# Optimization experiments

Measured on AMD Instinct MI355X. Metric: run time of the kernel, lower is better.

## Reference

```python
import jax, jax.numpy as jnp
import numpy as np

N = 2048
NODE_DIM = 128
HID = 128
HID2 = max(HID // 2, 4)  # 64
NUM_EDGE_TYPES = 1
TEMPERATURE = 1.0
LN_EPS = 1e-5


def setup_inputs() -> dict:
    key = jax.random.key(0)
    ks = jax.random.split(key, 12)
    s = lambda fan_in: 1.0 / np.sqrt(fan_in)
    inp = {
        "node_features": jax.random.normal(ks[0], (N, NODE_DIM), dtype=jnp.float32),
        # node_transform: Linear(node_dim, hidden)
        "Wt": jax.random.uniform(ks[1], (NODE_DIM, HID), jnp.float32, -s(NODE_DIM), s(NODE_DIM)),
        "bt": jax.random.uniform(ks[2], (HID,), jnp.float32, -s(NODE_DIM), s(NODE_DIM)),
        # edge_mlp Linear(2*hidden, hidden)
        "W1": jax.random.uniform(ks[3], (2 * HID, HID), jnp.float32, -s(2 * HID), s(2 * HID)),
        "b1": jax.random.uniform(ks[4], (HID,), jnp.float32, -s(2 * HID), s(2 * HID)),
        # LayerNorm(hidden)
        "ln_g": jnp.ones((HID,), jnp.float32),
        "ln_b": jnp.zeros((HID,), jnp.float32),
        # Linear(hidden, hidden//2)
        "W2": jax.random.uniform(ks[5], (HID, HID2), jnp.float32, -s(HID), s(HID)),
        "b2": jax.random.uniform(ks[6], (HID2,), jnp.float32, -s(HID), s(HID)),
        # Linear(hidden//2, num_edge_types)
        "W3": jax.random.uniform(ks[7], (HID2, NUM_EDGE_TYPES), jnp.float32, -s(HID2), s(HID2)),
        "b3": jax.random.uniform(ks[8], (NUM_EDGE_TYPES,), jnp.float32, -s(HID2), s(HID2)),
    }
    return inp


def reference(node_features, Wt, bt, W1, b1, ln_g, ln_b, W2, b2, W3, b3):
    n = node_features.shape[0]
    # node transform + relu: [n, hid]
    h = jax.nn.relu(node_features @ Wt + bt)
    # upper-triangular pair indices (i < j), matching the python loop order
    idx_i, idx_j = jnp.triu_indices(n, k=1)
    # gather + concat: [n_pairs, 2*hid]
    pair_feats = jnp.concatenate([h[idx_i], h[idx_j]], axis=1)
    # MLP: linear -> LN -> relu -> (dropout=identity in eval) -> linear -> relu -> linear
    z = pair_feats @ W1 + b1
    mu = jnp.mean(z, axis=-1, keepdims=True)
    var = jnp.mean((z - mu) ** 2, axis=-1, keepdims=True)
    z = (z - mu) * jax.lax.rsqrt(var + LN_EPS) * ln_g + ln_b
    z = jax.nn.relu(z)
    z = jax.nn.relu(z @ W2 + b2)
    logits = z @ W3 + b3  # [n_pairs, 1]
    probs = jax.nn.sigmoid(logits / max(1e-6, TEMPERATURE))
    pair_index = jnp.stack([idx_i, idx_j], axis=0)  # [2, n_pairs]
    p = probs.squeeze(1)
    soft_adj = jnp.zeros((n, n), dtype=probs.dtype)
    soft_adj = soft_adj.at[idx_i, idx_j].set(p).at[idx_j, idx_i].set(p)
    return probs, pair_index, soft_adj
```

## Files before the change

kernel.cpp:

```cpp
#include <hip/hip_runtime.h>
#include <math.h>

#define NN 2048
#define HID 128
#define HID2 64
#define NP ((NN*(NN-1))/2)

typedef _Float16 f16x8 __attribute__((ext_vector_type(8)));
typedef float    f32x4 __attribute__((ext_vector_type(4)));

__global__ __launch_bounds__(128) void precompute_AB(
    const float* __restrict__ X, const float* __restrict__ Wt, const float* __restrict__ bt,
    const float* __restrict__ W1, const float* __restrict__ b1,
    _Float16* __restrict__ Ah, _Float16* __restrict__ Bp,
    float2* __restrict__ sa, float2* __restrict__ sb)
{
    __shared__ float x_s[HID];
    __shared__ float h_s[HID];
    __shared__ float red[2][4];
    const int row = blockIdx.x;
    const int c = threadIdx.x;
    x_s[c] = X[row*HID + c];
    __syncthreads();
    float hc = bt[c];
    #pragma unroll 8
    for (int k = 0; k < HID; ++k) hc = fmaf(x_s[k], Wt[k*HID + c], hc);
    h_s[c] = fmaxf(hc, 0.f);
    __syncthreads();
    float a = b1[c];
    float bsum = 0.f;
    #pragma unroll 8
    for (int k = 0; k < HID; ++k) {
        float hk = h_s[k];
        a    = fmaf(hk, W1[k*HID + c], a);
        bsum = fmaf(hk, W1[(HID + k)*HID + c], bsum);
    }
    const _Float16 ah = (_Float16)a;
    const _Float16 bh = (_Float16)bsum;
    Ah[row*HID + c] = ah;
    {
        const int ks = c >> 5, g4 = (c >> 3) & 3, e = c & 7;
        Bp[(((size_t)(row >> 4)*4 + ks)*64 + g4*16 + (row & 15))*8 + e] = bh;
    }
    const float ar = (float)ah;
    const float br = (float)bh;
    float r0 = ar, r1 = ar*ar, r2 = br, r3 = br*br;
    #pragma unroll
    for (int m = 1; m <= 32; m <<= 1) {
        r0 += __shfl_xor(r0, m); r1 += __shfl_xor(r1, m);
        r2 += __shfl_xor(r2, m); r3 += __shfl_xor(r3, m);
    }
    if ((c & 63) == 0) {
        red[c >> 6][0] = r0; red[c >> 6][1] = r1; red[c >> 6][2] = r2; red[c >> 6][3] = r3;
    }
    __syncthreads();
    if (c == 0) {
        sa[row] = make_float2(red[0][0] + red[1][0], red[0][1] + red[1][1]);
        sb[row] = make_float2(red[0][2] + red[1][2], red[0][3] + red[1][3]);
    }
}

__global__ __launch_bounds__(256) void pack_W2(const float* __restrict__ W2,
                                               const float* __restrict__ ln_g,
                                               const float* __restrict__ ln_b,
                                               _Float16* __restrict__ W2p,
                                               _Float16* __restrict__ ghl,
                                               _Float16* __restrict__ lhl)
{
    const int t = threadIdx.x;
    if (t < HID) { ghl[t] = (_Float16)ln_g[t]; lhl[t] = (_Float16)ln_b[t]; }
    for (int fs = t; fs < 16*64; fs += 256) {
        const int frag = fs >> 6, lane = fs & 63;
        const int ks = frag >> 2, nt = frag & 3;
        const int kbase = ks*32 + (lane >> 4)*8;
        const int col   = nt*16 + (lane & 15);
        #pragma unroll
        for (int e = 0; e < 8; ++e)
            W2p[fs*8 + e] = (_Float16)W2[(kbase + e)*HID2 + col];
    }
}

__global__ __launch_bounds__(256) void fill_pi(float* __restrict__ pi)
{
    const int i = blockIdx.x;
    const size_t off = (size_t)i*(NN-1) - (size_t)i*(i-1)/2;
    const int cnt = NN - 1 - i;
    for (int t = threadIdx.x; t < cnt; t += 256) {
        pi[off + t]      = (float)i;
        pi[NP + off + t] = (float)(i + 1 + t);
    }
}

__global__ __launch_bounds__(256, 3) void pairs_mfma(
    const _Float16* __restrict__ Ah, const _Float16* __restrict__ Bp,
    const float2* __restrict__ sa, const float2* __restrict__ sb,
    const _Float16* __restrict__ ghl, const _Float16* __restrict__ lhl,
    const _Float16* __restrict__ W2p, const float* __restrict__ b2,
    const float* __restrict__ W3, const float* __restrict__ b3,
    float* __restrict__ out)
{
    __shared__ f16x8 w2s[16*64];

    {
        const f16x8* __restrict__ W2v = (const f16x8*)W2p;
        #pragma unroll
        for (int t = 0; t < 4; ++t)
            w2s[t*256 + threadIdx.x] = W2v[t*256 + threadIdx.x];
    }

    int t = blockIdx.x;
    int q = 0, base = 0;
    while (q < 7 && t >= base + 256*(8 - q)) { base += 256*(8 - q); ++q; }
    const int idx = t - base;
    const int den = 8 - q;
    const int i  = (q << 8) + idx / den;
    const int jb = q + idx % den;

    __syncthreads();

    const int w    = threadIdx.x >> 6;
    const int lane = threadIdx.x & 63;
    const int jw0  = (jb << 8) + (w << 6);
    if (jw0 + 63 < i) return;

    const int p16 = lane & 15;
    const int g4  = lane >> 4;

    f16x8 abf[4], gh[4], lh[4];
    #pragma unroll
    for (int ks = 0; ks < 4; ++ks) {
        const int kb = ks*32 + g4*8;
        abf[ks] = *(const f16x8*)(Ah + (size_t)i*HID + kb);
        gh[ks]  = *(const f16x8*)(ghl + kb);
        lh[ks]  = *(const f16x8*)(lhl + kb);
    }
    const float2 sav = sa[i];

    const f16x8* __restrict__ Bpv = (const f16x8*)Bp;

    float parts[4];

    f16x8 bcur[4], bnxt[4];
    {
        const size_t fb = ((size_t)(jw0 >> 4))*4;
        #pragma unroll
        for (int ks = 0; ks < 4; ++ks) bcur[ks] = Bpv[(fb + ks)*64 + lane];
    }

    #pragma unroll
    for (int s = 0; s < 4; ++s) {
        if (s < 3) {
            const size_t fbn = ((size_t)((jw0 + (s+1)*16) >> 4))*4;
            #pragma unroll
            for (int ks = 0; ks < 4; ++ks) bnxt[ks] = Bpv[(fbn + ks)*64 + lane];
        }
        const int j16 = jw0 + s*16;

        f32x4 d0 = (f32x4){0.f,0.f,0.f,0.f};
        f32x4 d1 = (f32x4){0.f,0.f,0.f,0.f};
        f32x4 d2 = (f32x4){0.f,0.f,0.f,0.f};
        f32x4 d3 = (f32x4){0.f,0.f,0.f,0.f};
        d0 = __builtin_amdgcn_mfma_f32_16x16x32_f16(abf[0], bcur[0], d0, 0, 0, 0);
        d1 = __builtin_amdgcn_mfma_f32_16x16x32_f16(abf[1], bcur[1], d1, 0, 0, 0);
        d2 = __builtin_amdgcn_mfma_f32_16x16x32_f16(abf[2], bcur[2], d2, 0, 0, 0);
        d3 = __builtin_amdgcn_mfma_f32_16x16x32_f16(abf[3], bcur[3], d3, 0, 0, 0);

        const float2 sbv = sb[j16 + p16];
        const float dd   = (d0[0] + d1[0]) + (d2[0] + d3[0]);
        const float mu   = (sav.x + sbv.x) * (1.f/HID);
        const float ez2  = (sav.y + sbv.y + 2.f*dd) * (1.f/HID);
        const float rstd = rsqrtf(ez2 - mu*mu + 1e-5f);
        const float v    = -mu * rstd;

        const _Float16 rh = (_Float16)rstd;
        const _Float16 vh = (_Float16)v;
        const f16x8 zero8 = {};

        f32x4 acc[4];
        #pragma unroll
        for (int nt = 0; nt < 4; ++nt) acc[nt] = *(const f32x4*)(b2 + nt*16 + g4*4);

        #pragma unroll
        for (int ks = 0; ks < 4; ++ks) {
            f16x8 z  = abf[ks] + bcur[ks];
            f16x8 qq = z * rh + vh;
            f16x8 af = __builtin_elementwise_max(gh[ks] * qq + lh[ks], zero8);
            #pragma unroll
            for (int nt = 0; nt < 4; ++nt)
                acc[nt] = __builtin_amdgcn_mfma_f32_16x16x32_f16(w2s[(ks*4 + nt)*64 + lane], af, acc[nt], 0, 0, 0);
        }

        float part = 0.f;
        #pragma unroll
        for (int nt = 0; nt < 4; ++nt) {
            f32x4 w3v = *(const f32x4*)(W3 + nt*16 + g4*4);
            #pragma unroll
            for (int r = 0; r < 4; ++r)
                part = fmaf(fmaxf(acc[nt][r], 0.f), w3v[r], part);
        }
        part += __shfl_xor(part, 16);
        part += __shfl_xor(part, 32);
        parts[s] = part;

        if (s < 3) {
            #pragma unroll
            for (int ks = 0; ks < 4; ++ks) bcur[ks] = bnxt[ks];
        }
    }

    const int sq = lane >> 4;
    float x = parts[0];
    x = (sq == 1) ? parts[1] : x;
    x = (sq == 2) ? parts[2] : x;
    x = (sq == 3) ? parts[3] : x;

    float* probs = out;
    float* adj   = out + 3*(size_t)NP;
    const int j = jw0 + lane;
    if (j == i) {
        adj[(size_t)i*NN + i] = 0.f;
    } else if (j > i) {
        const float pr = 1.f / (1.f + __expf(-(x + b3[0])));
        const int kpair = i*(NN-1) - (i*(i-1))/2 + (j - i - 1);
        probs[kpair] = pr;
        adj[(size_t)i*NN + j] = pr;
        adj[(size_t)j*NN + i] = pr;
    }
}

extern "C" void kernel_launch(void* const* d_in, const int* in_sizes, int n_in,
                              void* d_out, int out_size, void* d_ws, size_t ws_size,
                              hipStream_t stream) {
    const float* X    = (const float*)d_in[0];
    const float* Wt   = (const float*)d_in[1];
    const float* bt   = (const float*)d_in[2];
    const float* W1   = (const float*)d_in[3];
    const float* b1   = (const float*)d_in[4];
    const float* ln_g = (const float*)d_in[5];
    const float* ln_b = (const float*)d_in[6];
    const float* W2   = (const float*)d_in[7];
    const float* b2   = (const float*)d_in[8];
    const float* W3   = (const float*)d_in[9];
    const float* b3   = (const float*)d_in[10];
    float* out = (float*)d_out;

    float2*    sa  = (float2*)d_ws;
    float2*    sb  = sa + NN;
    _Float16*  Ah  = (_Float16*)(sb + NN);
    _Float16*  Bp  = Ah + (size_t)NN * HID;
    _Float16*  W2p = Bp + (size_t)NN * HID;
    _Float16*  ghl = W2p + 16*64*8;
    _Float16*  lhl = ghl + HID;

    precompute_AB<<<NN, HID, 0, stream>>>(X, Wt, bt, W1, b1, Ah, Bp, sa, sb);
    pack_W2<<<1, 256, 0, stream>>>(W2, ln_g, ln_b, W2p, ghl, lhl);
    fill_pi<<<NN-1, 256, 0, stream>>>(out + NP);

    const int nblk = 256 * 36;
    pairs_mfma<<<nblk, 256, 0, stream>>>(Ah, Bp, sa, sb, ghl, lhl, W2p, b2, W3, b3, out);
}
```

Baseline: 101.9 us.

## Fuse pair-index fill into pair kernel and software-pipeline dot MFMAs

Removes the separate fill_pi kernel and has the pair kernel write the i/j index values next to each probability, which saves a launch and a second pass over the output. The dot-product MFMAs for the next 16-column step are now issued one step ahead, so they overlap with the current step's LayerNorm and second-layer work. The final W3 reduction uses packed 2-wide float max/FMA. The cost is more register pressure and extra scattered stores inside the main kernel.

```diff
diff --git a/kernel.cpp b/kernel.cpp
--- a/kernel.cpp
+++ b/kernel.cpp
@@ -8,6 +8,7 @@
 
 typedef _Float16 f16x8 __attribute__((ext_vector_type(8)));
 typedef float    f32x4 __attribute__((ext_vector_type(4)));
+typedef float    f32x2 __attribute__((ext_vector_type(2)));
 
 __global__ __launch_bounds__(128) void precompute_AB(
     const float* __restrict__ X, const float* __restrict__ Wt, const float* __restrict__ bt,
@@ -80,17 +81,6 @@
     }
 }
 
-__global__ __launch_bounds__(256) void fill_pi(float* __restrict__ pi)
-{
-    const int i = blockIdx.x;
-    const size_t off = (size_t)i*(NN-1) - (size_t)i*(i-1)/2;
-    const int cnt = NN - 1 - i;
-    for (int t = threadIdx.x; t < cnt; t += 256) {
-        pi[off + t]      = (float)i;
-        pi[NP + off + t] = (float)(i + 1 + t);
-    }
-}
-
 __global__ __launch_bounds__(256, 3) void pairs_mfma(
     const _Float16* __restrict__ Ah, const _Float16* __restrict__ Bp,
     const float2* __restrict__ sa, const float2* __restrict__ sb,
@@ -146,6 +136,12 @@
         #pragma unroll
         for (int ks = 0; ks < 4; ++ks) bcur[ks] = Bpv[(fb + ks)*64 + lane];
     }
+    f32x4 dc[4];
+    #pragma unroll
+    for (int c = 0; c < 4; ++c) {
+        dc[c] = (f32x4){0.f,0.f,0.f,0.f};
+        dc[c] = __builtin_amdgcn_mfma_f32_16x16x32_f16(abf[c], bcur[c], dc[c], 0, 0, 0);
+    }
 
     #pragma unroll
     for (int s = 0; s < 4; ++s) {
@@ -156,22 +152,22 @@
         }
         const int j16 = jw0 + s*16;
 
-        f32x4 d0 = (f32x4){0.f,0.f,0.f,0.f};
-        f32x4 d1 = (f32x4){0.f,0.f,0.f,0.f};
-        f32x4 d2 = (f32x4){0.f,0.f,0.f,0.f};
-        f32x4 d3 = (f32x4){0.f,0.f,0.f,0.f};
-        d0 = __builtin_amdgcn_mfma_f32_16x16x32_f16(abf[0], bcur[0], d0, 0, 0, 0);
-        d1 = __builtin_amdgcn_mfma_f32_16x16x32_f16(abf[1], bcur[1], d1, 0, 0, 0);
-        d2 = __builtin_amdgcn_mfma_f32_16x16x32_f16(abf[2], bcur[2], d2, 0, 0, 0);
-        d3 = __builtin_amdgcn_mfma_f32_16x16x32_f16(abf[3], bcur[3], d3, 0, 0, 0);
-
         const float2 sbv = sb[j16 + p16];
-        const float dd   = (d0[0] + d1[0]) + (d2[0] + d3[0]);
+        const float dd   = (dc[0][0] + dc[1][0]) + (dc[2][0] + dc[3][0]);
         const float mu   = (sav.x + sbv.x) * (1.f/HID);
         const float ez2  = (sav.y + sbv.y + 2.f*dd) * (1.f/HID);
         const float rstd = rsqrtf(ez2 - mu*mu + 1e-5f);
         const float v    = -mu * rstd;
 
+        f32x4 dn[4];
+        if (s < 3) {
+            #pragma unroll
+            for (int c = 0; c < 4; ++c) {
+                dn[c] = (f32x4){0.f,0.f,0.f,0.f};
+                dn[c] = __builtin_amdgcn_mfma_f32_16x16x32_f16(abf[c], bnxt[c], dn[c], 0, 0, 0);
+            }
+        }
+
         const _Float16 rh = (_Float16)rstd;
         const _Float16 vh = (_Float16)v;
         const f16x8 zero8 = {};
@@ -190,14 +186,17 @@
                 acc[nt] = __builtin_amdgcn_mfma_f32_16x16x32_f16(w2s[(ks*4 + nt)*64 + lane], af, acc[nt], 0, 0, 0);
         }
 
-        float part = 0.f;
+        f32x2 pv = (f32x2){0.f, 0.f};
+        const f32x2 z2 = (f32x2){0.f, 0.f};
         #pragma unroll
         for (int nt = 0; nt < 4; ++nt) {
-            f32x4 w3v = *(const f32x4*)(W3 + nt*16 + g4*4);
-            #pragma unroll
-            for (int r = 0; r < 4; ++r)
-                part = fmaf(fmaxf(acc[nt][r], 0.f), w3v[r], part);
-        }
+            const f32x2* w3p = (const f32x2*)(W3 + nt*16 + g4*4);
+            f32x2 a0 = (f32x2){acc[nt][0], acc[nt][1]};
+            f32x2 a1 = (f32x2){acc[nt][2], acc[nt][3]};
+            pv = __builtin_elementwise_max(a0, z2) * w3p[0] + pv;
+            pv = __builtin_elementwise_max(a1, z2) * w3p[1] + pv;
+        }
+        float part = pv[0] + pv[1];
         part += __shfl_xor(part, 16);
         part += __shfl_xor(part, 32);
         parts[s] = part;
@@ -205,6 +204,8 @@
         if (s < 3) {
             #pragma unroll
             for (int ks = 0; ks < 4; ++ks) bcur[ks] = bnxt[ks];
+            #pragma unroll
+            for (int c = 0; c < 4; ++c) dc[c] = dn[c];
         }
     }
 
@@ -215,6 +216,7 @@
     x = (sq == 3) ? parts[3] : x;
 
     float* probs = out;
+    float* pi    = out + NP;
     float* adj   = out + 3*(size_t)NP;
     const int j = jw0 + lane;
     if (j == i) {
@@ -222,7 +224,9 @@
     } else if (j > i) {
         const float pr = 1.f / (1.f + __expf(-(x + b3[0])));
         const int kpair = i*(NN-1) - (i*(i-1))/2 + (j - i - 1);
-        probs[kpair] = pr;
+        probs[kpair]    = pr;
+        pi[kpair]       = (float)i;
+        pi[NP + kpair]  = (float)j;
         adj[(size_t)i*NN + j] = pr;
         adj[(size_t)j*NN + i] = pr;
     }
@@ -254,7 +258,6 @@
 
     precompute_AB<<<NN, HID, 0, stream>>>(X, Wt, bt, W1, b1, Ah, Bp, sa, sb);
     pack_W2<<<1, 256, 0, stream>>>(W2, ln_g, ln_b, W2p, ghl, lhl);
-    fill_pi<<<NN-1, 256, 0, stream>>>(out + NP);
 
     const int nblk = 256 * 36;
     pairs_mfma<<<nblk, 256, 0, stream>>>(Ah, Bp, sa, sb, ghl, lhl, W2p, b2, W3, b3, out);
```

Result: faster. 96.12 us (-5.7%).
